# Kernel tuning notes

Hardware: AMD Instinct MI355X
Metric: run time of the kernel (lower is better)

## Reference

```python
import jax, jax.numpy as jnp
import numpy as np

N, M, D = 8, 512, 64
B, H, W = 8192, 1, 1


def setup_inputs() -> dict:
    key = jax.random.key(0)
    k1, k2, k3 = jax.random.split(key, 3)
    x = jax.random.normal(k1, (B, N * D, H, W), dtype=jnp.float32)
    # nn.init.uniform_(embedding, -1/M, 1/M)
    embedding = jax.random.uniform(k2, (N, M, D), dtype=jnp.float32,
                                   minval=-1.0 / M, maxval=1.0 / M)
    # uniform base noise for Gumbel sampling (avoid exact 0)
    u = jax.random.uniform(k3, (N, B, H, W, M), dtype=jnp.float32,
                           minval=1e-6, maxval=1.0)
    tau = jnp.ones((1,), dtype=jnp.float32)
    return {"x": x, "embedding": embedding, "u": u, "tau": tau}


def reference(x, embedding, u, tau):
    n, m, d = embedding.shape
    b, c, h, w = x.shape
    # (B, N*D, H, W) -> (N, B*H*W, D)
    xr = x.reshape(b, n, d, h, w).transpose(1, 0, 3, 4, 2).reshape(n, b * h * w, d)
    e_sq = jnp.sum(embedding ** 2, axis=2)[:, None, :]          # (N, 1, M)
    x_sq = jnp.sum(xr ** 2, axis=2, keepdims=True)              # (N, BHW, 1)
    distances = e_sq + x_sq - 2.0 * jnp.einsum('nbd,nmd->nbm', xr, embedding)
    logits = -distances.reshape(n, b, h, w, m)
    # RelaxedOneHotCategorical normalizes logits to log-probs
    log_probs = jax.nn.log_softmax(logits, axis=-1)
    probs = jnp.exp(log_probs)
    # rsample: softmax((logits + gumbel) / tau); shift-invariant so log_probs ok
    gumbels = -jnp.log(-jnp.log(u))
    samples = jax.nn.softmax((log_probs + gumbels) / tau[0], axis=-1).reshape(n, -1, m)
    quantized = jnp.einsum('nbm,nmd->nbd', samples, embedding).reshape(n, b, 1, 1, d)
    logM = jnp.log(jnp.asarray(m, dtype=x.dtype))
    KL = jnp.where(probs == 0, jnp.zeros_like(probs), probs * (log_probs + logM))
    KL = KL.sum(axis=(0, 2, 3, 4)).mean()
    avg_probs = samples.mean(axis=1)                            # (N, M)
    perplexity = jnp.exp(-jnp.sum(avg_probs * jnp.log(avg_probs + 1e-10), axis=-1))
    ret_logits = jnp.transpose(log_probs, (1, 0, 4, 2, 3))      # (B, N, M, H, W)
    quantized = jnp.transpose(quantized, (1, 0, 4, 2, 3))       # (B, N, D, 1, 1)
    return (quantized, KL, perplexity.sum(), ret_logits)
```

## Files before the change

### kernel.cpp

```cpp
#include <hip/hip_runtime.h>
#include <stdint.h>

typedef short short8 __attribute__((ext_vector_type(8)));
typedef float float4v __attribute__((ext_vector_type(4)));
typedef unsigned long long ull;

#define R2      65536
#define LDS_SZ  81920

__device__ __forceinline__ unsigned cvtpk(float a, float b){
  unsigned d;
  asm("v_cvt_pk_bf16_f32 %0, %1, %2" : "=v"(d) : "v"(a), "v"(b));
  return d;
}
__device__ __forceinline__ unsigned short f2bf(float f){
  unsigned u = __float_as_uint(f);
  return (unsigned short)((u + 0x7FFFu + ((u >> 16) & 1u)) >> 16);
}

template<int OFF>
__device__ __forceinline__ ull tr16(unsigned a){
  ull d;
  asm volatile("ds_read_b64_tr_b16 %0, %1 offset:%c2" : "=v"(d) : "v"(a), "i"(OFF));
  return d;
}
__device__ __forceinline__ short8 mk8(ull lo, ull hi){
  union { ull q[2]; short8 v; } u; u.q[0] = lo; u.q[1] = hi; return u.v;
}

extern "C" __global__ void __launch_bounds__(512, 4)
vq_main(const float* __restrict__ gx, const float* __restrict__ ge,
        const float* __restrict__ gu, const float* __restrict__ gtau,
        float* __restrict__ gq, float* __restrict__ glg,
        float* __restrict__ ws_avg, float* __restrict__ ws_kl)
{
  extern __shared__ char smem[];
  const int tid = threadIdx.x;
  const int n   = blockIdx.x >> 6;
  const int b0  = (blockIdx.x & 63) * 128;

  float esq_reg = 0.f;
  {
    const int m = tid;
    const float* src = ge + (size_t)(n * 512 + m) * 64;
    char* dst = smem + m * 128;
    const unsigned sw = (unsigned)((m & 7) << 4);
#pragma unroll
    for (int c = 0; c < 8; ++c) {
      float4 a = *(const float4*)(src + c * 8);
      float4 b = *(const float4*)(src + c * 8 + 4);
      esq_reg += a.x*a.x + a.y*a.y + a.z*a.z + a.w*a.w
               + b.x*b.x + b.y*b.y + b.z*b.z + b.w*b.w;
      uint4 v = { cvtpk(a.x, a.y), cvtpk(a.z, a.w), cvtpk(b.x, b.y), cvtpk(b.z, b.w) };
      *(uint4*)(dst + (((unsigned)(c * 16)) ^ sw)) = v;
    }
  }
  {
    const int r = tid >> 2, qq = tid & 3;
    const float* src = gx + (size_t)(b0 + r) * 512 + n * 64 + qq * 16;
    char* dst = smem + R2 + r * 128;
    const unsigned sw = (unsigned)((r & 7) << 4);
#pragma unroll
    for (int h = 0; h < 2; ++h) {
      float4 a = *(const float4*)(src + h * 8);
      float4 b = *(const float4*)(src + h * 8 + 4);
      uint4 v = { cvtpk(a.x, a.y), cvtpk(a.z, a.w), cvtpk(b.x, b.y), cvtpk(b.z, b.w) };
      *(uint4*)(dst + (((unsigned)((qq * 2 + h) * 16)) ^ sw)) = v;
    }
  }
  __syncthreads();

  const int lane = tid & 63;
  const int w    = tid >> 6;
  const int l15  = lane & 15;
  const int kg   = lane >> 4;
  const unsigned swl = (unsigned)((l15 & 7) << 4);

  const char* xrow = smem + R2 + (w * 16 + l15) * 128;
  const short8 xb0 = *(const short8*)(xrow + (((unsigned)(kg * 16)) ^ swl));
  const short8 xb1 = *(const short8*)(xrow + (((unsigned)(64 + kg * 16)) ^ swl));
  __syncthreads();
  ((float*)(smem + R2))[tid] = esq_reg;
  __syncthreads();

  const char* erow = smem + l15 * 128;
  const unsigned eo0 = ((unsigned)(kg * 16)) ^ swl;
  const unsigned eo1 = ((unsigned)(64 + kg * 16)) ^ swl;
  const float* esqp = (const float*)(smem + R2);

  const float invtau = 1.0f / gtau[0];
  const float4* up4 = (const float4*)(gu + (size_t)n * 4194304
                     + (size_t)(b0 + w * 16 + l15) * 512 + kg * 4);

  float Z = 0.f, Wk = 0.f, Z2 = 0.f;
  {
    float4 Pa = up4[0], Pb = up4[4], Pc = up4[8], Pd = up4[12];
#pragma unroll
    for (int t = 0; t < 32; ++t) {
      short8 eb0 = *(const short8*)(erow + t * 2048 + eo0);
      short8 eb1 = *(const short8*)(erow + t * 2048 + eo1);
      float4v d = (float4v){0.f, 0.f, 0.f, 0.f};
      d = __builtin_amdgcn_mfma_f32_16x16x32_bf16(eb0, xb0, d, 0, 0, 0);
      d = __builtin_amdgcn_mfma_f32_16x16x32_bf16(eb1, xb1, d, 0, 0, 0);
      const float4 eq = *(const float4*)(esqp + t * 16 + kg * 4);
      const float s0 = 2.f * d[0] - eq.x;
      const float s1 = 2.f * d[1] - eq.y;
      const float s2 = 2.f * d[2] - eq.z;
      const float s3 = 2.f * d[3] - eq.w;
      const float e0 = __expf(s0), e1 = __expf(s1), e2 = __expf(s2), e3 = __expf(s3);
      Z  += e0 + e1 + e2 + e3;
      Wk += e0 * s0 + e1 * s1 + e2 * s2 + e3 * s3;
      const float4 uu = Pa;
      Pa = Pb; Pb = Pc; Pc = Pd;
      if (t < 28) Pd = up4[(t + 4) * 4];
      const float g0 = -__logf(-__logf(uu.x));
      const float g1 = -__logf(-__logf(uu.y));
      const float g2 = -__logf(-__logf(uu.z));
      const float g3 = -__logf(-__logf(uu.w));
      Z2 += __expf((s0 + g0) * invtau) + __expf((s1 + g1) * invtau)
          + __expf((s2 + g2) * invtau) + __expf((s3 + g3) * invtau);
    }
  }
  Z  += __shfl_xor(Z, 16);  Z  += __shfl_xor(Z, 32);
  Wk += __shfl_xor(Wk, 16); Wk += __shfl_xor(Wk, 32);
  Z2 += __shfl_xor(Z2, 16); Z2 += __shfl_xor(Z2, 32);
  const float lse = __logf(Z);
  const float logM = 6.2383246250395075f;
  float klrow = Wk / Z - lse + logM;
  const float rz2 = 1.0f / Z2;

  float4v* lp4 = (float4v*)(glg + (size_t)(b0 + w * 16 + l15) * 4096 + n * 512 + kg * 4);
  ushort* sampw = (ushort*)(smem + R2 + 8192 + w * 1024);
  const char* sampc = (const char*)sampw;
  const unsigned trA = (unsigned)(uintptr_t)sampw
                     + (unsigned)(kg * 128 + (l15 >> 2) * 32 + (l15 & 3) * 8);
  const int mrow = kg * 4 + (l15 >> 2);
  const unsigned ebase = (unsigned)(uintptr_t)smem + (unsigned)(mrow * 128);
  const unsigned msw = ((unsigned)(mrow & 7)) << 4;
  unsigned trB0 = ebase + ((unsigned)(  0 + (l15 & 3) * 8) ^ msw);
  unsigned trB1 = ebase + ((unsigned)( 32 + (l15 & 3) * 8) ^ msw);
  unsigned trB2 = ebase + ((unsigned)( 64 + (l15 & 3) * 8) ^ msw);
  unsigned trB3 = ebase + ((unsigned)( 96 + (l15 & 3) * 8) ^ msw);

  float4v qacc0 = (float4v){0.f,0.f,0.f,0.f};
  float4v qacc1 = (float4v){0.f,0.f,0.f,0.f};
  float4v qacc2 = (float4v){0.f,0.f,0.f,0.f};
  float4v qacc3 = (float4v){0.f,0.f,0.f,0.f};
  float4v avgA  = (float4v){0.f,0.f,0.f,0.f};
  float4v avgB  = (float4v){0.f,0.f,0.f,0.f};

  float4 P0 = up4[0], P1 = up4[4], P2 = up4[8], P3 = up4[12];
#pragma unroll
  for (int c = 0; c < 16; ++c) {
    const float4 cu0 = P0, cu1 = P1;
    P0 = P2; P1 = P3;
    if (c < 14) { P2 = up4[(2 * c + 4) * 4]; P3 = up4[(2 * c + 5) * 4]; }
#pragma unroll
    for (int th = 0; th < 2; ++th) {
      const int t = c * 2 + th;
      short8 eb0 = *(const short8*)(erow + t * 2048 + eo0);
      short8 eb1 = *(const short8*)(erow + t * 2048 + eo1);
      float4v d = (float4v){0.f, 0.f, 0.f, 0.f};
      d = __builtin_amdgcn_mfma_f32_16x16x32_bf16(eb0, xb0, d, 0, 0, 0);
      d = __builtin_amdgcn_mfma_f32_16x16x32_bf16(eb1, xb1, d, 0, 0, 0);
      const float4 eq = *(const float4*)(esqp + t * 16 + kg * 4);
      const float s0 = 2.f * d[0] - eq.x;
      const float s1 = 2.f * d[1] - eq.y;
      const float s2 = 2.f * d[2] - eq.z;
      const float s3 = 2.f * d[3] - eq.w;
      float4v lpv = { s0 - lse, s1 - lse, s2 - lse, s3 - lse };
      lp4[t * 4] = lpv;
      const float4 uu = (th == 0) ? cu0 : cu1;
      const float g0 = -__logf(-__logf(uu.x));
      const float g1 = -__logf(-__logf(uu.y));
      const float g2 = -__logf(-__logf(uu.z));
      const float g3 = -__logf(-__logf(uu.w));
      const float y0 = __expf((s0 + g0) * invtau) * rz2;
      const float y1 = __expf((s1 + g1) * invtau) * rz2;
      const float y2 = __expf((s2 + g2) * invtau) * rz2;
      const float y3 = __expf((s3 + g3) * invtau) * rz2;
      sampw[(th * 16 + kg * 4 + 0) * 16 + l15] = f2bf(y0);
      sampw[(th * 16 + kg * 4 + 1) * 16 + l15] = f2bf(y1);
      sampw[(th * 16 + kg * 4 + 2) * 16 + l15] = f2bf(y2);
      sampw[(th * 16 + kg * 4 + 3) * 16 + l15] = f2bf(y3);
    }
    asm volatile("s_waitcnt lgkmcnt(0)" ::: "memory");
    __builtin_amdgcn_sched_barrier(0);
    const short8 avA = *(const short8*)(sampc + l15 * 32 + (kg & 1) * 16);
    const short8 avB = *(const short8*)(sampc + 512 + l15 * 32 + (kg & 1) * 16);
    ull alo = tr16<0>(trA),  ahi = tr16<512>(trA);
    ull b0l = tr16<0>(trB0), b0h = tr16<2048>(trB0);
    ull b1l = tr16<0>(trB1), b1h = tr16<2048>(trB1);
    ull b2l = tr16<0>(trB2), b2h = tr16<2048>(trB2);
    ull b3l = tr16<0>(trB3), b3h = tr16<2048>(trB3);
    asm volatile("s_waitcnt lgkmcnt(0)" ::: "memory");
    __builtin_amdgcn_sched_barrier(0);
    const unsigned onv = ((l15 == c) && (kg < 2)) ? 0x3F803F80u : 0u;
    union { unsigned u[4]; short8 v; } bs;
    bs.u[0] = onv; bs.u[1] = onv; bs.u[2] = onv; bs.u[3] = onv;
    short8 aa = mk8(alo, ahi);
    qacc0 = __builtin_amdgcn_mfma_f32_16x16x32_bf16(aa, mk8(b0l, b0h), qacc0, 0, 0, 0);
    qacc1 = __builtin_amdgcn_mfma_f32_16x16x32_bf16(aa, mk8(b1l, b1h), qacc1, 0, 0, 0);
    qacc2 = __builtin_amdgcn_mfma_f32_16x16x32_bf16(aa, mk8(b2l, b2h), qacc2, 0, 0, 0);
    qacc3 = __builtin_amdgcn_mfma_f32_16x16x32_bf16(aa, mk8(b3l, b3h), qacc3, 0, 0, 0);
    avgA  = __builtin_amdgcn_mfma_f32_16x16x32_bf16(avA, bs.v, avgA, 0, 0, 0);
    avgB  = __builtin_amdgcn_mfma_f32_16x16x32_bf16(avB, bs.v, avgB, 0, 0, 0);
    trB0 += 4096; trB1 += 4096; trB2 += 4096; trB3 += 4096;
  }

  {
    const size_t qb = (size_t)(b0 + w * 16 + kg * 4) * 512 + n * 64 + l15;
#pragma unroll
    for (int j = 0; j < 4; ++j) {
      gq[qb + (size_t)j * 512 +  0] = qacc0[j];
      gq[qb + (size_t)j * 512 + 16] = qacc1[j];
      gq[qb + (size_t)j * 512 + 32] = qacc2[j];
      gq[qb + (size_t)j * 512 + 48] = qacc3[j];
    }
  }

  klrow += __shfl_xor(klrow, 1); klrow += __shfl_xor(klrow, 2);
  klrow += __shfl_xor(klrow, 4); klrow += __shfl_xor(klrow, 8);

  __syncthreads();
  float* avgl = (float*)(smem + R2);
  float* kls  = (float*)smem;
  if (lane == 0) kls[w] = klrow;
  *(float4v*)(avgl + w * 512 + l15 * 32 + kg * 4)      = avgA;
  *(float4v*)(avgl + w * 512 + l15 * 32 + 16 + kg * 4) = avgB;
  __syncthreads();
  {
    float s = 0.f;
#pragma unroll
    for (int ww = 0; ww < 8; ++ww) s += avgl[ww * 512 + tid];
    ws_avg[(size_t)blockIdx.x * 512 + tid] = s;
    if (tid == 0) {
      float k = 0.f;
#pragma unroll
      for (int i = 0; i < 8; ++i) k += kls[i];
      ws_kl[blockIdx.x] = k;
    }
  }
}

extern "C" __global__ void __launch_bounds__(512)
vq_fin(const float* __restrict__ ws_avg, const float* __restrict__ ws_kl,
       float* __restrict__ scal)
{
  __shared__ float red[8];
  const int tid = threadIdx.x, lane = tid & 63, w = tid >> 6;
  float pps = 0.f;
  for (int n = 0; n < 8; ++n) {
    float s = 0.f;
    for (int bt = 0; bt < 64; ++bt) s += ws_avg[(size_t)(n * 64 + bt) * 512 + tid];
    const float avg = s * (1.0f / 8192.0f);
    float term = avg * __logf(avg + 1e-10f);
#pragma unroll
    for (int o = 1; o < 64; o <<= 1) term += __shfl_xor(term, o);
    __syncthreads();
    if (lane == 0) red[w] = term;
    __syncthreads();
    if (tid == 0) {
      float tt = 0.f;
#pragma unroll
      for (int i = 0; i < 8; ++i) tt += red[i];
      pps += __expf(-tt);
    }
  }
  float kv = ws_kl[tid];
#pragma unroll
  for (int o = 1; o < 64; o <<= 1) kv += __shfl_xor(kv, o);
  __syncthreads();
  if (lane == 0) red[w] = kv;
  __syncthreads();
  if (tid == 0) {
    float k = 0.f;
#pragma unroll
    for (int i = 0; i < 8; ++i) k += red[i];
    scal[0] = k * (1.0f / 8192.0f);
    scal[1] = pps;
  }
}

extern "C" void kernel_launch(void* const* d_in, const int* in_sizes, int n_in,
                              void* d_out, int out_size, void* d_ws, size_t ws_size,
                              hipStream_t stream)
{
  const float* gx = (const float*)d_in[0];
  const float* ge = (const float*)d_in[1];
  const float* gu = (const float*)d_in[2];
  const float* gt = (const float*)d_in[3];
  float* out  = (float*)d_out;
  float* gq   = out;
  float* scal = out + 4194304;
  float* glg  = out + 4194306;
  float* ws_avg = (float*)d_ws;
  float* ws_kl  = ws_avg + 512 * 512;

  (void)hipFuncSetAttribute((const void*)vq_main,
                            hipFuncAttributeMaxDynamicSharedMemorySize, LDS_SZ);
  vq_main<<<dim3(512), dim3(512), LDS_SZ, stream>>>(gx, ge, gu, gt, gq, glg, ws_avg, ws_kl);
  vq_fin<<<dim3(1), dim3(512), 0, stream>>>(ws_avg, ws_kl, scal);
}
```

Before: 125.8 us.

## Cache unnormalized bf16 Gumbel weights in registers and simplify tau=1 path

The first sweep now computes the unnormalized Gumbel-softmax weights once, packs them to bf16 in 64 registers per lane, and reuses them in the second sweep instead of reloading u and recomputing double logs and exps. For tau==1 it uses the algebraic identity exp(s - log(-log u)) = e^s / (-log u), replacing an exp and a log with a reciprocal and reusing e^s. Divisions become hardware rcp. This removes the second pass's global reads of u and its transcendental work, at the cost of much higher register pressure, which may reduce occupancy or cause spills. Z2 is now summed from the bf16-rounded values, so the normalisation matches the stored samples.

```diff
diff --git a/kernel.cpp b/kernel.cpp
--- a/kernel.cpp
+++ b/kernel.cpp
@@ -3,6 +3,7 @@
 
 typedef short short8 __attribute__((ext_vector_type(8)));
 typedef float float4v __attribute__((ext_vector_type(4)));
+typedef unsigned uint8x __attribute__((ext_vector_type(8)));
 typedef unsigned long long ull;
 
 #define R2      65536
@@ -13,10 +14,8 @@
   asm("v_cvt_pk_bf16_f32 %0, %1, %2" : "=v"(d) : "v"(a), "v"(b));
   return d;
 }
-__device__ __forceinline__ unsigned short f2bf(float f){
-  unsigned u = __float_as_uint(f);
-  return (unsigned short)((u + 0x7FFFu + ((u >> 16) & 1u)) >> 16);
-}
+__device__ __forceinline__ float bfLO(unsigned r){ return __uint_as_float(r << 16); }
+__device__ __forceinline__ float bfHI(unsigned r){ return __uint_as_float(r & 0xffff0000u); }
 
 template<int OFF>
 __device__ __forceinline__ ull tr16(unsigned a){
@@ -88,46 +87,64 @@
   const unsigned eo1 = ((unsigned)(64 + kg * 16)) ^ swl;
   const float* esqp = (const float*)(smem + R2);
 
-  const float invtau = 1.0f / gtau[0];
+  const float tauv = gtau[0];
+  const bool tau1 = (tauv == 1.0f);
+  const float invtau = 1.0f / tauv;
   const float4* up4 = (const float4*)(gu + (size_t)n * 4194304
                      + (size_t)(b0 + w * 16 + l15) * 512 + kg * 4);
 
+  uint8x syv[8];
   float Z = 0.f, Wk = 0.f, Z2 = 0.f;
-  {
-    float4 Pa = up4[0], Pb = up4[4], Pc = up4[8], Pd = up4[12];
-#pragma unroll
-    for (int t = 0; t < 32; ++t) {
-      short8 eb0 = *(const short8*)(erow + t * 2048 + eo0);
-      short8 eb1 = *(const short8*)(erow + t * 2048 + eo1);
-      float4v d = (float4v){0.f, 0.f, 0.f, 0.f};
-      d = __builtin_amdgcn_mfma_f32_16x16x32_bf16(eb0, xb0, d, 0, 0, 0);
-      d = __builtin_amdgcn_mfma_f32_16x16x32_bf16(eb1, xb1, d, 0, 0, 0);
-      const float4 eq = *(const float4*)(esqp + t * 16 + kg * 4);
-      const float s0 = 2.f * d[0] - eq.x;
-      const float s1 = 2.f * d[1] - eq.y;
-      const float s2 = 2.f * d[2] - eq.z;
-      const float s3 = 2.f * d[3] - eq.w;
-      const float e0 = __expf(s0), e1 = __expf(s1), e2 = __expf(s2), e3 = __expf(s3);
-      Z  += e0 + e1 + e2 + e3;
-      Wk += e0 * s0 + e1 * s1 + e2 * s2 + e3 * s3;
-      const float4 uu = Pa;
-      Pa = Pb; Pb = Pc; Pc = Pd;
-      if (t < 28) Pd = up4[(t + 4) * 4];
-      const float g0 = -__logf(-__logf(uu.x));
-      const float g1 = -__logf(-__logf(uu.y));
-      const float g2 = -__logf(-__logf(uu.z));
-      const float g3 = -__logf(-__logf(uu.w));
-      Z2 += __expf((s0 + g0) * invtau) + __expf((s1 + g1) * invtau)
-          + __expf((s2 + g2) * invtau) + __expf((s3 + g3) * invtau);
-    }
-  }
+
+#define SWEEP1(YEXPR0, YEXPR1, YEXPR2, YEXPR3)                                 \
+  {                                                                            \
+    float4 Pa = up4[0], Pb = up4[4], Pc = up4[8], Pd = up4[12];                \
+    _Pragma("unroll")                                                          \
+    for (int t = 0; t < 32; ++t) {                                             \
+      short8 eb0 = *(const short8*)(erow + t * 2048 + eo0);                    \
+      short8 eb1 = *(const short8*)(erow + t * 2048 + eo1);                    \
+      float4v d = (float4v){0.f, 0.f, 0.f, 0.f};                               \
+      d = __builtin_amdgcn_mfma_f32_16x16x32_bf16(eb0, xb0, d, 0, 0, 0);       \
+      d = __builtin_amdgcn_mfma_f32_16x16x32_bf16(eb1, xb1, d, 0, 0, 0);       \
+      const float4 eq = *(const float4*)(esqp + t * 16 + kg * 4);              \
+      const float s0 = 2.f * d[0] - eq.x;                                      \
+      const float s1 = 2.f * d[1] - eq.y;                                      \
+      const float s2 = 2.f * d[2] - eq.z;                                      \
+      const float s3 = 2.f * d[3] - eq.w;                                      \
+      const float e0 = __expf(s0), e1 = __expf(s1);                            \
+      const float e2 = __expf(s2), e3 = __expf(s3);                            \
+      Z  += (e0 + e1) + (e2 + e3);                                             \
+      Wk += e0 * s0 + e1 * s1 + e2 * s2 + e3 * s3;                             \
+      const float4 uu = Pa;                                                    \
+      Pa = Pb; Pb = Pc; Pc = Pd;                                               \
+      if (t < 28) Pd = up4[(t + 4) * 4];                                       \
+      const float l0 = -__logf(uu.x), l1 = -__logf(uu.y);                      \
+      const float l2 = -__logf(uu.z), l3 = -__logf(uu.w);                      \
+      const float y0 = (YEXPR0), y1 = (YEXPR1);                                \
+      const float y2 = (YEXPR2), y3 = (YEXPR3);                                \
+      const unsigned pk0 = cvtpk(y0, y1);                                      \
+      const unsigned pk1 = cvtpk(y2, y3);                                      \
+      syv[t >> 2][2 * (t & 3)]     = pk0;                                      \
+      syv[t >> 2][2 * (t & 3) + 1] = pk1;                                      \
+      Z2 += (bfLO(pk0) + bfHI(pk0)) + (bfLO(pk1) + bfHI(pk1));                 \
+    }                                                                          \
+  }
+
+  if (tau1) {
+    SWEEP1(e0 * __builtin_amdgcn_rcpf(l0), e1 * __builtin_amdgcn_rcpf(l1),
+           e2 * __builtin_amdgcn_rcpf(l2), e3 * __builtin_amdgcn_rcpf(l3))
+  } else {
+    SWEEP1(__expf((s0 - __logf(l0)) * invtau), __expf((s1 - __logf(l1)) * invtau),
+           __expf((s2 - __logf(l2)) * invtau), __expf((s3 - __logf(l3)) * invtau))
+  }
+
   Z  += __shfl_xor(Z, 16);  Z  += __shfl_xor(Z, 32);
   Wk += __shfl_xor(Wk, 16); Wk += __shfl_xor(Wk, 32);
   Z2 += __shfl_xor(Z2, 16); Z2 += __shfl_xor(Z2, 32);
   const float lse = __logf(Z);
   const float logM = 6.2383246250395075f;
-  float klrow = Wk / Z - lse + logM;
-  const float rz2 = 1.0f / Z2;
+  float klrow = Wk * __builtin_amdgcn_rcpf(Z) - lse + logM;
+  const float rz2 = __builtin_amdgcn_rcpf(Z2);
 
   float4v* lp4 = (float4v*)(glg + (size_t)(b0 + w * 16 + l15) * 4096 + n * 512 + kg * 4);
   ushort* sampw = (ushort*)(smem + R2 + 8192 + w * 1024);
@@ -149,12 +166,8 @@
   float4v avgA  = (float4v){0.f,0.f,0.f,0.f};
   float4v avgB  = (float4v){0.f,0.f,0.f,0.f};
 
-  float4 P0 = up4[0], P1 = up4[4], P2 = up4[8], P3 = up4[12];
 #pragma unroll
   for (int c = 0; c < 16; ++c) {
-    const float4 cu0 = P0, cu1 = P1;
-    P0 = P2; P1 = P3;
-    if (c < 14) { P2 = up4[(2 * c + 4) * 4]; P3 = up4[(2 * c + 5) * 4]; }
 #pragma unroll
     for (int th = 0; th < 2; ++th) {
       const int t = c * 2 + th;
@@ -164,25 +177,17 @@
       d = __builtin_amdgcn_mfma_f32_16x16x32_bf16(eb0, xb0, d, 0, 0, 0);
       d = __builtin_amdgcn_mfma_f32_16x16x32_bf16(eb1, xb1, d, 0, 0, 0);
       const float4 eq = *(const float4*)(esqp + t * 16 + kg * 4);
-      const float s0 = 2.f * d[0] - eq.x;
-      const float s1 = 2.f * d[1] - eq.y;
-      const float s2 = 2.f * d[2] - eq.z;
-      const float s3 = 2.f * d[3] - eq.w;
-      float4v lpv = { s0 - lse, s1 - lse, s2 - lse, s3 - lse };
+      float4v lpv = { 2.f * d[0] - eq.x - lse, 2.f * d[1] - eq.y - lse,
+                      2.f * d[2] - eq.z - lse, 2.f * d[3] - eq.w - lse };
       lp4[t * 4] = lpv;
-      const float4 uu = (th == 0) ? cu0 : cu1;
-      const float g0 = -__logf(-__logf(uu.x));
-      const float g1 = -__logf(-__logf(uu.y));
-      const float g2 = -__logf(-__logf(uu.z));
-      const float g3 = -__logf(-__logf(uu.w));
-      const float y0 = __expf((s0 + g0) * invtau) * rz2;
-      const float y1 = __expf((s1 + g1) * invtau) * rz2;
-      const float y2 = __expf((s2 + g2) * invtau) * rz2;
-      const float y3 = __expf((s3 + g3) * invtau) * rz2;
-      sampw[(th * 16 + kg * 4 + 0) * 16 + l15] = f2bf(y0);
-      sampw[(th * 16 + kg * 4 + 1) * 16 + l15] = f2bf(y1);
-      sampw[(th * 16 + kg * 4 + 2) * 16 + l15] = f2bf(y2);
-      sampw[(th * 16 + kg * 4 + 3) * 16 + l15] = f2bf(y3);
+      const unsigned pk0 = syv[t >> 2][2 * (t & 3)];
+      const unsigned pk1 = syv[t >> 2][2 * (t & 3) + 1];
+      const unsigned q0 = cvtpk(bfLO(pk0) * rz2, bfHI(pk0) * rz2);
+      const unsigned q1 = cvtpk(bfLO(pk1) * rz2, bfHI(pk1) * rz2);
+      sampw[(th * 16 + kg * 4 + 0) * 16 + l15] = (ushort)q0;
+      sampw[(th * 16 + kg * 4 + 1) * 16 + l15] = (ushort)(q0 >> 16);
+      sampw[(th * 16 + kg * 4 + 2) * 16 + l15] = (ushort)q1;
+      sampw[(th * 16 + kg * 4 + 3) * 16 + l15] = (ushort)(q1 >> 16);
     }
     asm volatile("s_waitcnt lgkmcnt(0)" ::: "memory");
     __builtin_amdgcn_sched_barrier(0);
```

After: 213.2 us. 69.5% more time.

## Stash unnormalized Gumbel-softmax samples in workspace to avoid rereading noise

Applied to the files above, without the earlier changes.

Adds a variant kernel that computes the unnormalized sample weights in the first sweep, packs them to bf16 and writes them to a global workspace buffer, so the second sweep reloads 8-byte packed values instead of re-reading the fp32 uniform noise and recomputing the log/exp chain. For tau equal to 1 it also rewrites exp(s - log(-log u)) as exp(s) times a reciprocal of -log u, reusing the exp already computed for the partition function. Divisions are replaced with hardware reciprocals. It needs a large workspace, falls back to the old kernel otherwise, and adds an extra global write and read plus bf16 rounding before normalization.

```diff
diff --git a/kernel.cpp b/kernel.cpp
--- a/kernel.cpp
+++ b/kernel.cpp
@@ -17,6 +17,8 @@
   unsigned u = __float_as_uint(f);
   return (unsigned short)((u + 0x7FFFu + ((u >> 16) & 1u)) >> 16);
 }
+__device__ __forceinline__ float bfLO(unsigned r){ return __uint_as_float(r << 16); }
+__device__ __forceinline__ float bfHI(unsigned r){ return __uint_as_float(r & 0xffff0000u); }
 
 template<int OFF>
 __device__ __forceinline__ ull tr16(unsigned a){
@@ -28,65 +30,248 @@
   union { ull q[2]; short8 v; } u; u.q[0] = lo; u.q[1] = hi; return u.v;
 }
 
+#define VQ_PROLOGUE                                                            \
+  extern __shared__ char smem[];                                               \
+  const int tid = threadIdx.x;                                                 \
+  const int n   = blockIdx.x >> 6;                                             \
+  const int b0  = (blockIdx.x & 63) * 128;                                     \
+  float esq_reg = 0.f;                                                         \
+  {                                                                            \
+    const int m = tid;                                                         \
+    const float* src = ge + (size_t)(n * 512 + m) * 64;                        \
+    char* dst = smem + m * 128;                                                \
+    const unsigned sw = (unsigned)((m & 7) << 4);                              \
+    _Pragma("unroll")                                                          \
+    for (int c = 0; c < 8; ++c) {                                              \
+      float4 a = *(const float4*)(src + c * 8);                                \
+      float4 b = *(const float4*)(src + c * 8 + 4);                            \
+      esq_reg += a.x*a.x + a.y*a.y + a.z*a.z + a.w*a.w                         \
+               + b.x*b.x + b.y*b.y + b.z*b.z + b.w*b.w;                        \
+      uint4 v = { cvtpk(a.x, a.y), cvtpk(a.z, a.w),                            \
+                  cvtpk(b.x, b.y), cvtpk(b.z, b.w) };                          \
+      *(uint4*)(dst + (((unsigned)(c * 16)) ^ sw)) = v;                        \
+    }                                                                          \
+  }                                                                            \
+  {                                                                            \
+    const int r = tid >> 2, qq = tid & 3;                                      \
+    const float* src = gx + (size_t)(b0 + r) * 512 + n * 64 + qq * 16;         \
+    char* dst = smem + R2 + r * 128;                                           \
+    const unsigned sw = (unsigned)((r & 7) << 4);                              \
+    _Pragma("unroll")                                                          \
+    for (int h = 0; h < 2; ++h) {                                              \
+      float4 a = *(const float4*)(src + h * 8);                                \
+      float4 b = *(const float4*)(src + h * 8 + 4);                            \
+      uint4 v = { cvtpk(a.x, a.y), cvtpk(a.z, a.w),                            \
+                  cvtpk(b.x, b.y), cvtpk(b.z, b.w) };                          \
+      *(uint4*)(dst + (((unsigned)((qq * 2 + h) * 16)) ^ sw)) = v;             \
+    }                                                                          \
+  }                                                                            \
+  __syncthreads();                                                             \
+  const int lane = tid & 63;                                                   \
+  const int w    = tid >> 6;                                                   \
+  const int l15  = lane & 15;                                                  \
+  const int kg   = lane >> 4;                                                  \
+  const unsigned swl = (unsigned)((l15 & 7) << 4);                             \
+  const char* xrow = smem + R2 + (w * 16 + l15) * 128;                         \
+  const short8 xb0 = *(const short8*)(xrow + (((unsigned)(kg * 16)) ^ swl));   \
+  const short8 xb1 = *(const short8*)(xrow + (((unsigned)(64 + kg * 16)) ^ swl)); \
+  __syncthreads();                                                             \
+  ((float*)(smem + R2))[tid] = esq_reg;                                        \
+  __syncthreads();                                                             \
+  const char* erow = smem + l15 * 128;                                         \
+  const unsigned eo0 = ((unsigned)(kg * 16)) ^ swl;                            \
+  const unsigned eo1 = ((unsigned)(64 + kg * 16)) ^ swl;                       \
+  const float* esqp = (const float*)(smem + R2);
+
+#define VQ_EPILOGUE                                                            \
+  {                                                                            \
+    const size_t qb = (size_t)(b0 + w * 16 + kg * 4) * 512 + n * 64 + l15;     \
+    _Pragma("unroll")                                                          \
+    for (int j = 0; j < 4; ++j) {                                              \
+      gq[qb + (size_t)j * 512 +  0] = qacc0[j];                                \
+      gq[qb + (size_t)j * 512 + 16] = qacc1[j];                                \
+      gq[qb + (size_t)j * 512 + 32] = qacc2[j];                                \
+      gq[qb + (size_t)j * 512 + 48] = qacc3[j];                                \
+    }                                                                          \
+  }                                                                            \
+  klrow += __shfl_xor(klrow, 1); klrow += __shfl_xor(klrow, 2);                \
+  klrow += __shfl_xor(klrow, 4); klrow += __shfl_xor(klrow, 8);                \
+  __syncthreads();                                                             \
+  float* avgl = (float*)(smem + R2);                                           \
+  float* kls  = (float*)smem;                                                  \
+  if (lane == 0) kls[w] = klrow;                                               \
+  *(float4v*)(avgl + w * 512 + l15 * 32 + kg * 4)      = avgA;                 \
+  *(float4v*)(avgl + w * 512 + l15 * 32 + 16 + kg * 4) = avgB;                 \
+  __syncthreads();                                                             \
+  {                                                                            \
+    float s = 0.f;                                                             \
+    _Pragma("unroll")                                                          \
+    for (int ww = 0; ww < 8; ++ww) s += avgl[ww * 512 + tid];                  \
+    ws_avg[(size_t)blockIdx.x * 512 + tid] = s;                                \
+    if (tid == 0) {                                                            \
+      float k = 0.f;                                                           \
+      _Pragma("unroll")                                                        \
+      for (int i = 0; i < 8; ++i) k += kls[i];                                 \
+      ws_kl[blockIdx.x] = k;                                                   \
+    }                                                                          \
+  }
+
+#define PHASE_B_TAIL(cvar)                                                     \
+    asm volatile("s_waitcnt lgkmcnt(0)" ::: "memory");                         \
+    __builtin_amdgcn_sched_barrier(0);                                         \
+    const short8 avA = *(const short8*)(sampc + l15 * 32 + (kg & 1) * 16);     \
+    const short8 avB = *(const short8*)(sampc + 512 + l15 * 32 + (kg & 1) * 16); \
+    ull alo = tr16<0>(trA),  ahi = tr16<512>(trA);                             \
+    ull b0l = tr16<0>(trB0), b0h = tr16<2048>(trB0);                           \
+    ull b1l = tr16<0>(trB1), b1h = tr16<2048>(trB1);                           \
+    ull b2l = tr16<0>(trB2), b2h = tr16<2048>(trB2);                           \
+    ull b3l = tr16<0>(trB3), b3h = tr16<2048>(trB3);                           \
+    asm volatile("s_waitcnt lgkmcnt(0)" ::: "memory");                         \
+    __builtin_amdgcn_sched_barrier(0);                                         \
+    const unsigned onv = ((l15 == (cvar)) && (kg < 2)) ? 0x3F803F80u : 0u;     \
+    union { unsigned u[4]; short8 v; } bs;                                     \
+    bs.u[0] = onv; bs.u[1] = onv; bs.u[2] = onv; bs.u[3] = onv;                \
+    short8 aa = mk8(alo, ahi);                                                 \
+    qacc0 = __builtin_amdgcn_mfma_f32_16x16x32_bf16(aa, mk8(b0l, b0h), qacc0, 0, 0, 0); \
+    qacc1 = __builtin_amdgcn_mfma_f32_16x16x32_bf16(aa, mk8(b1l, b1h), qacc1, 0, 0, 0); \
+    qacc2 = __builtin_amdgcn_mfma_f32_16x16x32_bf16(aa, mk8(b2l, b2h), qacc2, 0, 0, 0); \
+    qacc3 = __builtin_amdgcn_mfma_f32_16x16x32_bf16(aa, mk8(b3l, b3h), qacc3, 0, 0, 0); \
+    avgA  = __builtin_amdgcn_mfma_f32_16x16x32_bf16(avA, bs.v, avgA, 0, 0, 0); \
+    avgB  = __builtin_amdgcn_mfma_f32_16x16x32_bf16(avB, bs.v, avgB, 0, 0, 0); \
+    trB0 += 4096; trB1 += 4096; trB2 += 4096; trB3 += 4096;
+
+#define PHASE_B_DECLS                                                          \
+  ushort* sampw = (ushort*)(smem + R2 + 8192 + w * 1024);                      \
+  const char* sampc = (const char*)sampw;                                      \
+  const unsigned trA = (unsigned)(uintptr_t)sampw                              \
+                     + (unsigned)(kg * 128 + (l15 >> 2) * 32 + (l15 & 3) * 8); \
+  const int mrow = kg * 4 + (l15 >> 2);                                        \
+  const unsigned ebase = (unsigned)(uintptr_t)smem + (unsigned)(mrow * 128);   \
+  const unsigned msw = ((unsigned)(mrow & 7)) << 4;                            \
+  unsigned trB0 = ebase + ((unsigned)(  0 + (l15 & 3) * 8) ^ msw);             \
+  unsigned trB1 = ebase + ((unsigned)( 32 + (l15 & 3) * 8) ^ msw);             \
+  unsigned trB2 = ebase + ((unsigned)( 64 + (l15 & 3) * 8) ^ msw);             \
+  unsigned trB3 = ebase + ((unsigned)( 96 + (l15 & 3) * 8) ^ msw);             \
+  float4v qacc0 = (float4v){0.f,0.f,0.f,0.f};                                  \
+  float4v qacc1 = (float4v){0.f,0.f,0.f,0.f};                                  \
+  float4v qacc2 = (float4v){0.f,0.f,0.f,0.f};                                  \
+  float4v qacc3 = (float4v){0.f,0.f,0.f,0.f};                                  \
+  float4v avgA  = (float4v){0.f,0.f,0.f,0.f};                                  \
+  float4v avgB  = (float4v){0.f,0.f,0.f,0.f};
+
 extern "C" __global__ void __launch_bounds__(512, 4)
-vq_main(const float* __restrict__ gx, const float* __restrict__ ge,
-        const float* __restrict__ gu, const float* __restrict__ gtau,
-        float* __restrict__ gq, float* __restrict__ glg,
-        float* __restrict__ ws_avg, float* __restrict__ ws_kl)
+vq_main_ws(const float* __restrict__ gx, const float* __restrict__ ge,
+           const float* __restrict__ gu, const float* __restrict__ gtau,
+           float* __restrict__ gq, float* __restrict__ glg,
+           ull* __restrict__ gy,
+           float* __restrict__ ws_avg, float* __restrict__ ws_kl)
 {
-  extern __shared__ char smem[];
-  const int tid = threadIdx.x;
-  const int n   = blockIdx.x >> 6;
-  const int b0  = (blockIdx.x & 63) * 128;
-
-  float esq_reg = 0.f;
-  {
-    const int m = tid;
-    const float* src = ge + (size_t)(n * 512 + m) * 64;
-    char* dst = smem + m * 128;
-    const unsigned sw = (unsigned)((m & 7) << 4);
-#pragma unroll
-    for (int c = 0; c < 8; ++c) {
-      float4 a = *(const float4*)(src + c * 8);
-      float4 b = *(const float4*)(src + c * 8 + 4);
-      esq_reg += a.x*a.x + a.y*a.y + a.z*a.z + a.w*a.w
-               + b.x*b.x + b.y*b.y + b.z*b.z + b.w*b.w;
-      uint4 v = { cvtpk(a.x, a.y), cvtpk(a.z, a.w), cvtpk(b.x, b.y), cvtpk(b.z, b.w) };
-      *(uint4*)(dst + (((unsigned)(c * 16)) ^ sw)) = v;
+  VQ_PROLOGUE
+
+  const float tauv = gtau[0];
+  const float invtau = 1.0f / tauv;
+  const bool tau1 = (tauv == 1.0f);
+  const float4* up4 = (const float4*)(gu + (size_t)n * 4194304
+                     + (size_t)(b0 + w * 16 + l15) * 512 + kg * 4);
+  ull* gyw = gy + ((size_t)blockIdx.x * 8 + w) * 2048;
+
+  float Z = 0.f, Wk = 0.f, Z2 = 0.f;
+
+#define SWEEP1(YE0, YE1, YE2, YE3)                                             \
+  {                                                                            \
+    float4 Pa = up4[0], Pb = up4[4], Pc = up4[8], Pd = up4[12];                \
+    _Pragma("unroll")                                                          \
+    for (int t = 0; t < 32; ++t) {                                             \
+      short8 eb0 = *(const short8*)(erow + t * 2048 + eo0);                    \
+      short8 eb1 = *(const short8*)(erow + t * 2048 + eo1);                    \
+      float4v d = (float4v){0.f, 0.f, 0.f, 0.f};                               \
+      d = __builtin_amdgcn_mfma_f32_16x16x32_bf16(eb0, xb0, d, 0, 0, 0);       \
+      d = __builtin_amdgcn_mfma_f32_16x16x32_bf16(eb1, xb1, d, 0, 0, 0);       \
+      const float4 eq = *(const float4*)(esqp + t * 16 + kg * 4);              \
+      const float s0 = 2.f * d[0] - eq.x;                                      \
+      const float s1 = 2.f * d[1] - eq.y;                                      \
+      const float s2 = 2.f * d[2] - eq.z;                                      \
+      const float s3 = 2.f * d[3] - eq.w;                                      \
+      const float e0 = __expf(s0), e1 = __expf(s1);                            \
+      const float e2 = __expf(s2), e3 = __expf(s3);                            \
+      Z  += (e0 + e1) + (e2 + e3);                                             \
+      Wk += e0 * s0 + e1 * s1 + e2 * s2 + e3 * s3;                             \
+      const float4 uu = Pa;                                                    \
+      Pa = Pb; Pb = Pc; Pc = Pd;                                               \
+      if (t < 28) Pd = up4[(t + 4) * 4];                                       \
+      const float l0 = -__logf(uu.x), l1 = -__logf(uu.y);                      \
+      const float l2 = -__logf(uu.z), l3 = -__logf(uu.w);                      \
+      const float y0 = (YE0), y1 = (YE1);                                      \
+      const float y2 = (YE2), y3 = (YE3);                                      \
+      const unsigned pk0 = cvtpk(y0, y1);                                      \
+      const unsigned pk1 = cvtpk(y2, y3);                                      \
+      gyw[t * 64 + lane] = (ull)pk0 | ((ull)pk1 << 32);                        \
+      Z2 += (y0 + y1) + (y2 + y3);                                             \
+    }                                                                          \
+  }
+
+  if (tau1) {
+    SWEEP1(e0 * __builtin_amdgcn_rcpf(l0), e1 * __builtin_amdgcn_rcpf(l1),
+           e2 * __builtin_amdgcn_rcpf(l2), e3 * __builtin_amdgcn_rcpf(l3))
+  } else {
+    SWEEP1(__expf((s0 - __logf(l0)) * invtau), __expf((s1 - __logf(l1)) * invtau),
+           __expf((s2 - __logf(l2)) * invtau), __expf((s3 - __logf(l3)) * invtau))
+  }
+#undef SWEEP1
+
+  Z  += __shfl_xor(Z, 16);  Z  += __shfl_xor(Z, 32);
+  Wk += __shfl_xor(Wk, 16); Wk += __shfl_xor(Wk, 32);
+  Z2 += __shfl_xor(Z2, 16); Z2 += __shfl_xor(Z2, 32);
+  const float lse = __logf(Z);
+  const float logM = 6.2383246250395075f;
+  float klrow = Wk * __builtin_amdgcn_rcpf(Z) - lse + logM;
+  const float rz2 = __builtin_amdgcn_rcpf(Z2);
+
+  asm volatile("s_waitcnt vmcnt(0)" ::: "memory");
+
+  float4v* lp4 = (float4v*)(glg + (size_t)(b0 + w * 16 + l15) * 4096 + n * 512 + kg * 4);
+  PHASE_B_DECLS
+
+  ull Ya[4] = { gyw[lane], gyw[64 + lane], gyw[128 + lane], gyw[192 + lane] };
+
+#pragma unroll
+  for (int c = 0; c < 16; ++c) {
+#pragma unroll
+    for (int th = 0; th < 2; ++th) {
+      const int t = c * 2 + th;
+      short8 eb0 = *(const short8*)(erow + t * 2048 + eo0);
+      short8 eb1 = *(const short8*)(erow + t * 2048 + eo1);
+      float4v d = (float4v){0.f, 0.f, 0.f, 0.f};
+      d = __builtin_amdgcn_mfma_f32_16x16x32_bf16(eb0, xb0, d, 0, 0, 0);
+      d = __builtin_amdgcn_mfma_f32_16x16x32_bf16(eb1, xb1, d, 0, 0, 0);
+      const float4 eq = *(const float4*)(esqp + t * 16 + kg * 4);
+      float4v lpv = { 2.f * d[0] - eq.x - lse, 2.f * d[1] - eq.y - lse,
+                      2.f * d[2] - eq.z - lse, 2.f * d[3] - eq.w - lse };
+      lp4[t * 4] = lpv;
+      const ull yc = Ya[t & 3];
+      if (t < 28) Ya[t & 3] = gyw[(t + 4) * 64 + lane];
+      const unsigned pk0 = (unsigned)yc;
+      const unsigned pk1 = (unsigned)(yc >> 32);
+      const unsigned q0 = cvtpk(bfLO(pk0) * rz2, bfHI(pk0) * rz2);
+      const unsigned q1 = cvtpk(bfLO(pk1) * rz2, bfHI(pk1) * rz2);
+      sampw[(th * 16 + kg * 4 + 0) * 16 + l15] = (ushort)q0;
+      sampw[(th * 16 + kg * 4 + 1) * 16 + l15] = (ushort)(q0 >> 16);
+      sampw[(th * 16 + kg * 4 + 2) * 16 + l15] = (ushort)q1;
+      sampw[(th * 16 + kg * 4 + 3) * 16 + l15] = (ushort)(q1 >> 16);
     }
-  }
-  {
-    const int r = tid >> 2, qq = tid & 3;
-    const float* src = gx + (size_t)(b0 + r) * 512 + n * 64 + qq * 16;
-    char* dst = smem + R2 + r * 128;
-    const unsigned sw = (unsigned)((r & 7) << 4);
-#pragma unroll
-    for (int h = 0; h < 2; ++h) {
-      float4 a = *(const float4*)(src + h * 8);
-      float4 b = *(const float4*)(src + h * 8 + 4);
-      uint4 v = { cvtpk(a.x, a.y), cvtpk(a.z, a.w), cvtpk(b.x, b.y), cvtpk(b.z, b.w) };
-      *(uint4*)(dst + (((unsigned)((qq * 2 + h) * 16)) ^ sw)) = v;
-    }
-  }
-  __syncthreads();
-
-  const int lane = tid & 63;
-  const int w    = tid >> 6;
-  const int l15  = lane & 15;
-  const int kg   = lane >> 4;
-  const unsigned swl = (unsigned)((l15 & 7) << 4);
-
-  const char* xrow = smem + R2 + (w * 16 + l15) * 128;
-  const short8 xb0 = *(const short8*)(xrow + (((unsigned)(kg * 16)) ^ swl));
-  const short8 xb1 = *(const short8*)(xrow + (((unsigned)(64 + kg * 16)) ^ swl));
-  __syncthreads();
-  ((float*)(smem + R2))[tid] = esq_reg;
-  __syncthreads();
-
-  const char* erow = smem + l15 * 128;
-  const unsigned eo0 = ((unsigned)(kg * 16)) ^ swl;
-  const unsigned eo1 = ((unsigned)(64 + kg * 16)) ^ swl;
-  const float* esqp = (const float*)(smem + R2);
+    PHASE_B_TAIL(c)
+  }
+
+  VQ_EPILOGUE
+}
+
+extern "C" __global__ void __launch_bounds__(512, 4)
+vq_main_fb(const float* __restrict__ gx, const float* __restrict__ ge,
+           const float* __restrict__ gu, const float* __restrict__ gtau,
+           float* __restrict__ gq, float* __restrict__ glg,
+           float* __restrict__ ws_avg, float* __restrict__ ws_kl)
+{
+  VQ_PROLOGUE
 
   const float invtau = 1.0f / gtau[0];
   const float4* up4 = (const float4*)(gu + (size_t)n * 4194304
@@ -108,7 +293,7 @@
       const float s2 = 2.f * d[2] - eq.z;
       const float s3 = 2.f * d[3] - eq.w;
       const float e0 = __expf(s0), e1 = __expf(s1), e2 = __expf(s2), e3 = __expf(s3);
-      Z  += e0 + e1 + e2 + e3;
+      Z  += (e0 + e1) + (e2 + e3);
       Wk += e0 * s0 + e1 * s1 + e2 * s2 + e3 * s3;
       const float4 uu = Pa;
       Pa = Pb; Pb = Pc; Pc = Pd;
@@ -126,28 +311,11 @@
   Z2 += __shfl_xor(Z2, 16); Z2 += __shfl_xor(Z2, 32);
   const float lse = __logf(Z);
   const float logM = 6.2383246250395075f;
-  float klrow = Wk / Z - lse + logM;
-  const float rz2 = 1.0f / Z2;
+  float klrow = Wk * __builtin_amdgcn_rcpf(Z) - lse + logM;
+  const float rz2 = __builtin_amdgcn_rcpf(Z2);
 
   float4v* lp4 = (float4v*)(glg + (size_t)(b0 + w * 16 + l15) * 4096 + n * 512 + kg * 4);
-  ushort* sampw = (ushort*)(smem + R2 + 8192 + w * 1024);
-  const char* sampc = (const char*)sampw;
-  const unsigned trA = (unsigned)(uintptr_t)sampw
-                     + (unsigned)(kg * 128 + (l15 >> 2) * 32 + (l15 & 3) * 8);
-  const int mrow = kg * 4 + (l15 >> 2);
-  const unsigned ebase = (unsigned)(uintptr_t)smem + (unsigned)(mrow * 128);
-  const unsigned msw = ((unsigned)(mrow & 7)) << 4;
-  unsigned trB0 = ebase + ((unsigned)(  0 + (l15 & 3) * 8) ^ msw);
-  unsigned trB1 = ebase + ((unsigned)( 32 + (l15 & 3) * 8) ^ msw);
-  unsigned trB2 = ebase + ((unsigned)( 64 + (l15 & 3) * 8) ^ msw);
-  unsigned trB3 = ebase + ((unsigned)( 96 + (l15 & 3) * 8) ^ msw);
-
-  float4v qacc0 = (float4v){0.f,0.f,0.f,0.f};
-  float4v qacc1 = (float4v){0.f,0.f,0.f,0.f};
-  float4v qacc2 = (float4v){0.f,0.f,0.f,0.f};
-  float4v qacc3 = (float4v){0.f,0.f,0.f,0.f};
-  float4v avgA  = (float4v){0.f,0.f,0.f,0.f};
-  float4v avgB  = (float4v){0.f,0.f,0.f,0.f};
+  PHASE_B_DECLS
 
   float4 P0 = up4[0], P1 = up4[4], P2 = up4[8], P3 = up4[12];
 #pragma unroll
@@ -184,63 +352,10 @@
       sampw[(th * 16 + kg * 4 + 2) * 16 + l15] = f2bf(y2);
       sampw[(th * 16 + kg * 4 + 3) * 16 + l15] = f2bf(y3);
     }
-    asm volatile("s_waitcnt lgkmcnt(0)" ::: "memory");
-    __builtin_amdgcn_sched_barrier(0);
-    const short8 avA = *(const short8*)(sampc + l15 * 32 + (kg & 1) * 16);
-    const short8 avB = *(const short8*)(sampc + 512 + l15 * 32 + (kg & 1) * 16);
-    ull alo = tr16<0>(trA),  ahi = tr16<512>(trA);
-    ull b0l = tr16<0>(trB0), b0h = tr16<2048>(trB0);
-    ull b1l = tr16<0>(trB1), b1h = tr16<2048>(trB1);
-    ull b2l = tr16<0>(trB2), b2h = tr16<2048>(trB2);
-    ull b3l = tr16<0>(trB3), b3h = tr16<2048>(trB3);
-    asm volatile("s_waitcnt lgkmcnt(0)" ::: "memory");
-    __builtin_amdgcn_sched_barrier(0);
-    const unsigned onv = ((l15 == c) && (kg < 2)) ? 0x3F803F80u : 0u;
-    union { unsigned u[4]; short8 v; } bs;
-    bs.u[0] = onv; bs.u[1] = onv; bs.u[2] = onv; bs.u[3] = onv;
-    short8 aa = mk8(alo, ahi);
-    qacc0 = __builtin_amdgcn_mfma_f32_16x16x32_bf16(aa, mk8(b0l, b0h), qacc0, 0, 0, 0);
-    qacc1 = __builtin_amdgcn_mfma_f32_16x16x32_bf16(aa, mk8(b1l, b1h), qacc1, 0, 0, 0);
-    qacc2 = __builtin_amdgcn_mfma_f32_16x16x32_bf16(aa, mk8(b2l, b2h), qacc2, 0, 0, 0);
-    qacc3 = __builtin_amdgcn_mfma_f32_16x16x32_bf16(aa, mk8(b3l, b3h), qacc3, 0, 0, 0);
-    avgA  = __builtin_amdgcn_mfma_f32_16x16x32_bf16(avA, bs.v, avgA, 0, 0, 0);
-    avgB  = __builtin_amdgcn_mfma_f32_16x16x32_bf16(avB, bs.v, avgB, 0, 0, 0);
-    trB0 += 4096; trB1 += 4096; trB2 += 4096; trB3 += 4096;
-  }
-
-  {
-    const size_t qb = (size_t)(b0 + w * 16 + kg * 4) * 512 + n * 64 + l15;
-#pragma unroll
-    for (int j = 0; j < 4; ++j) {
-      gq[qb + (size_t)j * 512 +  0] = qacc0[j];
-      gq[qb + (size_t)j * 512 + 16] = qacc1[j];
-      gq[qb + (size_t)j * 512 + 32] = qacc2[j];
-      gq[qb + (size_t)j * 512 + 48] = qacc3[j];
-    }
-  }
-
-  klrow += __shfl_xor(klrow, 1); klrow += __shfl_xor(klrow, 2);
-  klrow += __shfl_xor(klrow, 4); klrow += __shfl_xor(klrow, 8);
-
-  __syncthreads();
-  float* avgl = (float*)(smem + R2);
-  float* kls  = (float*)smem;
-  if (lane == 0) kls[w] = klrow;
-  *(float4v*)(avgl + w * 512 + l15 * 32 + kg * 4)      = avgA;
-  *(float4v*)(avgl + w * 512 + l15 * 32 + 16 + kg * 4) = avgB;
-  __syncthreads();
-  {
-    float s = 0.f;
-#pragma unroll
-    for (int ww = 0; ww < 8; ++ww) s += avgl[ww * 512 + tid];
-    ws_avg[(size_t)blockIdx.x * 512 + tid] = s;
-    if (tid == 0) {
-      float k = 0.f;
-#pragma unroll
-      for (int i = 0; i < 8; ++i) k += kls[i];
-      ws_kl[blockIdx.x] = k;
-    }
-  }
+    PHASE_B_TAIL(c)
+  }
+
+  VQ_EPILOGUE
 }
 
 extern "C" __global__ void __launch_bounds__(512)
@@ -294,11 +409,26 @@
   float* gq   = out;
   float* scal = out + 4194304;
   float* glg  = out + 4194306;
-  float* ws_avg = (float*)d_ws;
-  float* ws_kl  = ws_avg + 512 * 512;
-
-  (void)hipFuncSetAttribute((const void*)vq_main,
-                            hipFuncAttributeMaxDynamicSharedMemorySize, LDS_SZ);
-  vq_main<<<dim3(512), dim3(512), LDS_SZ, stream>>>(gx, ge, gu, gt, gq, glg, ws_avg, ws_kl);
-  vq_fin<<<dim3(1), dim3(512), 0, stream>>>(ws_avg, ws_kl, scal);
-}
+
+  const size_t GY_BYTES = (size_t)512 * 8 * 2048 * 8;
+  const size_t NEED = GY_BYTES + (size_t)512 * 512 * 4 + 2048;
+
+  if (ws_size >= NEED) {
+    ull*   gy     = (ull*)d_ws;
+    float* ws_avg = (float*)((char*)d_ws + GY_BYTES);
+    float* ws_kl  = ws_avg + 512 * 512;
+    (void)hipFuncSetAttribute((const void*)vq_main_ws,
+                              hipFuncAttributeMaxDynamicSharedMemorySize, LDS_SZ);
+    vq_main_ws<<<dim3(512), dim3(512), LDS_SZ, stream>>>(gx, ge, gu, gt, gq, glg,
+                                                         gy, ws_avg, ws_kl);
+    vq_fin<<<dim3(1), dim3(512), 0, stream>>>(ws_avg, ws_kl, scal);
+  } else {
+    float* ws_avg = (float*)d_ws;
+    float* ws_kl  = ws_avg + 512 * 512;
+    (void)hipFuncSetAttribute((const void*)vq_main_fb,
+                              hipFuncAttributeMaxDynamicSharedMemorySize, LDS_SZ);
+    vq_main_fb<<<dim3(512), dim3(512), LDS_SZ, stream>>>(gx, ge, gu, gt, gq, glg,
+                                                         ws_avg, ws_kl);
+    vq_fin<<<dim3(1), dim3(512), 0, stream>>>(ws_avg, ws_kl, scal);
+  }
+}
```

Measured after the change: 138.1 us. 9.7% more time.
